# Performance work log

Measured on AMD Instinct MI355X. Metric: run time of the kernel, lower is better.

The kernel has to match this reference:

```python
import jax, jax.numpy as jnp
import numpy as np

N_NODES = 50000


def _gcn_layer(x, src, dst, W, b, inv_deg):
    # gather src features, scatter-add into dst, right-normalize, then dense transform
    agg = jax.ops.segment_sum(x[src], dst, num_segments=N_NODES)  # [N, F]
    h = agg * inv_deg[:, None]
    return h @ W + b


def setup_inputs() -> dict:
    key = jax.random.key(0)
    ks = jax.random.split(key, 6)
    E = 800000
    x = jax.random.normal(ks[0], (N_NODES, 128), dtype=jnp.float32)
    src = jax.random.randint(ks[1], (E,), 0, N_NODES, dtype=jnp.int64)
    dst = jax.random.randint(ks[2], (E,), 0, N_NODES, dtype=jnp.int64)
    W1 = jax.random.normal(ks[3], (128, 128), dtype=jnp.float32) * (1.0 / np.sqrt(128))
    b1 = jnp.zeros((128,), dtype=jnp.float32)
    W2 = jax.random.normal(ks[4], (128, 64), dtype=jnp.float32) * (1.0 / np.sqrt(128))
    b2 = jnp.zeros((64,), dtype=jnp.float32)
    return {"x": x, "src": src, "dst": dst, "W1": W1, "b1": b1, "W2": W2, "b2": b2}


def reference(x, src, dst, W1, b1, W2, b2):
    # in-degree, clamped to 1 (DGL norm='right')
    deg = jax.ops.segment_sum(jnp.ones_like(dst, dtype=x.dtype), dst, num_segments=N_NODES)
    inv_deg = 1.0 / jnp.maximum(deg, 1.0)
    h = _gcn_layer(x, src, dst, W1, b1, inv_deg)
    h = jax.nn.relu(h)  # Dropout in eval mode == identity
    out = _gcn_layer(h, src, dst, W2, b2, inv_deg)
    return out
```

## Files before the change

### kernel.cpp

```cpp
#include <hip/hip_runtime.h>


constexpr int NNODES = 50000;
constexpr int NEDGES = 800000;
constexpr int NBUCKETS = (NNODES + 255) / 256;
constexpr int ABLOCKS = 200;
constexpr int PER = (NEDGES + ABLOCKS - 1) / ABLOCKS;
constexpr int NB_CAST = NNODES / 16;
constexpr int NB_PREP = (128 * 128 + 64 * 128 + 255) / 256;

constexpr size_t SZ_ROWSTART = 50048;
constexpr size_t SZ_INVDEG   = 50048;
constexpr size_t SZ_H        = (size_t)ABLOCKS * 256;
constexpr size_t SZ_LOFS     = (size_t)ABLOCKS * 256;
constexpr size_t SZ_CSR      = NEDGES;
constexpr size_t SZ_TMP      = NEDGES;
constexpr size_t SZ_WT1      = 128 * 128 / 2;
constexpr size_t SZ_WT2      = 64 * 128 / 2;
constexpr size_t SZ_SCALEX   = 50048;
constexpr size_t SZ_XQ       = (size_t)NNODES * 128 / 4;
constexpr size_t SZ_AGGH     = (size_t)NNODES * 128 / 2;
constexpr size_t SZ_Y2H      = (size_t)NNODES * 64 / 2;

constexpr size_t OFF_ROWSTART = 0;
constexpr size_t OFF_INVDEG   = OFF_ROWSTART + SZ_ROWSTART;
constexpr size_t OFF_H        = OFF_INVDEG   + SZ_INVDEG;
constexpr size_t OFF_LOFS     = OFF_H        + SZ_H;
constexpr size_t OFF_CSR      = OFF_LOFS     + SZ_LOFS;
constexpr size_t OFF_TMP      = OFF_CSR      + SZ_CSR;
constexpr size_t OFF_WT1      = OFF_TMP      + SZ_TMP;
constexpr size_t OFF_WT2      = OFF_WT1      + SZ_WT1;
constexpr size_t OFF_SCALEX   = OFF_WT2      + SZ_WT2;
constexpr size_t OFF_XQ       = OFF_SCALEX   + SZ_SCALEX;
constexpr size_t OFF_AGGH     = OFF_XQ       + SZ_XQ;
constexpr size_t OFF_Y2H      = OFF_AGGH     + SZ_AGGH;
constexpr size_t WS_WORDS     = OFF_Y2H      + SZ_Y2H;
static_assert(WS_WORDS < 11452800, "exceeds r7-proven workspace size");

typedef unsigned short ushortv8 __attribute__((ext_vector_type(8)));
typedef short bf16x8 __attribute__((ext_vector_type(8)));
typedef float f32x4 __attribute__((ext_vector_type(4)));
typedef signed char charv8 __attribute__((ext_vector_type(8)));
typedef signed char charv16 __attribute__((ext_vector_type(16)));

static __device__ __forceinline__ unsigned short f2bf(float f) {
    unsigned u = __float_as_uint(f);
    u += 0x7fff + ((u >> 16) & 1);
    return (unsigned short)(u >> 16);
}
static __device__ __forceinline__ float bf2f(unsigned short h) {
    return __uint_as_float((unsigned)h << 16);
}

__global__ __launch_bounds__(256) void setup_kernel(
    const int* __restrict__ src, const int* __restrict__ dst,
    unsigned* __restrict__ tmp, int* __restrict__ H, int* __restrict__ LOFS,
    const float* __restrict__ x, signed char* __restrict__ xq,
    float* __restrict__ scaleX,
    const float* __restrict__ W1, const float* __restrict__ W2,
    unsigned short* __restrict__ Wt1, unsigned short* __restrict__ Wt2)
{
    const int blk = blockIdx.x;
    const int t = threadIdx.x;
    if (blk < ABLOCKS) {
        __shared__ int cnt[256];
        __shared__ int ofs[256];
        __shared__ int cur[256];
        cnt[t] = 0;
        __syncthreads();
        const int lo = blk * PER;
        const int hi = min(lo + PER, NEDGES);
        for (int i = lo + t; i < hi; i += 256)
            atomicAdd(&cnt[dst[i] >> 8], 1);
        __syncthreads();
        ofs[t] = cnt[t];
        __syncthreads();
        #pragma unroll
        for (int off = 1; off < 256; off <<= 1) {
            const int o = (t >= off) ? ofs[t - off] : 0;
            __syncthreads();
            ofs[t] += o;
            __syncthreads();
        }
        const int excl = ofs[t] - cnt[t];
        cur[t] = excl;
        H[blk * 256 + t] = cnt[t];
        LOFS[blk * 256 + t] = excl;
        __syncthreads();
        for (int i = lo + t; i < hi; i += 256) {
            const int d = dst[i];
            const unsigned pk = ((unsigned)src[i] << 8) | (unsigned)(d & 255);
            const int pos = lo + atomicAdd(&cur[d >> 8], 1);
            tmp[pos] = pk;
        }
    } else if (blk < ABLOCKS + NB_CAST) {
        const int lane = t & 63;
        const int wave = t >> 6;
        const int row = (blk - ABLOCKS) * 16 + wave * 4 + (lane >> 4);
        const int ls = lane & 15;
        const float4* px =
            reinterpret_cast<const float4*>(x + (size_t)row * 128 + ls * 8);
        const float4 a = px[0], b = px[1];
        float m = fmaxf(
            fmaxf(fmaxf(fabsf(a.x), fabsf(a.y)), fmaxf(fabsf(a.z), fabsf(a.w))),
            fmaxf(fmaxf(fabsf(b.x), fabsf(b.y)), fmaxf(fabsf(b.z), fabsf(b.w))));
        #pragma unroll
        for (int msk = 1; msk < 16; msk <<= 1)
            m = fmaxf(m, __shfl_xor(m, msk, 16));
        const float rs = (m > 0.f) ? 127.0f / m : 0.f;
        charv8 q;
        q[0] = (signed char)__float2int_rn(a.x * rs);
        q[1] = (signed char)__float2int_rn(a.y * rs);
        q[2] = (signed char)__float2int_rn(a.z * rs);
        q[3] = (signed char)__float2int_rn(a.w * rs);
        q[4] = (signed char)__float2int_rn(b.x * rs);
        q[5] = (signed char)__float2int_rn(b.y * rs);
        q[6] = (signed char)__float2int_rn(b.z * rs);
        q[7] = (signed char)__float2int_rn(b.w * rs);
        *reinterpret_cast<charv8*>(xq + (size_t)row * 128 + ls * 8) = q;
        if (ls == 0) scaleX[row] = (m > 0.f) ? m / 127.0f : 0.f;
    } else {
        const int i = (blk - ABLOCKS - NB_CAST) * 256 + t;
        if (i < 128 * 128) {
            const int n = i >> 7, k = i & 127;
            Wt1[i] = f2bf(W1[k * 128 + n]);
        } else if (i < 128 * 128 + 64 * 128) {
            const int j = i - 128 * 128;
            const int n = j >> 7, k = j & 127;
            Wt2[j] = f2bf(W2[k * 64 + n]);
        }
    }
}

__global__ __launch_bounds__(256) void partB_kernel(
    const unsigned* __restrict__ tmp, const int* __restrict__ H,
    const int* __restrict__ LOFS, int* __restrict__ csr,
    int* __restrict__ rowStart, float* __restrict__ inv_deg, int nNodes)
{
    __shared__ int cs[256];
    __shared__ int s[256];
    __shared__ int epfx[256];
    __shared__ int base[256];
    __shared__ int cnt[256];
    __shared__ int fill[256];
    const int b = blockIdx.x;
    const int t = threadIdx.x;

    int sum = 0;
    for (int w = 0; w < ABLOCKS; ++w) sum += H[w * 256 + t];
    cs[t] = sum;
    s[t] = sum;
    __syncthreads();
    #pragma unroll
    for (int off = 1; off < 256; off <<= 1) {
        const int o = (t >= off) ? s[t - off] : 0;
        __syncthreads();
        s[t] += o;
        __syncthreads();
    }
    const int gbase = s[b] - cs[b];
    const int total = cs[b];
    __syncthreads();

    const int hv = (t < ABLOCKS) ? H[t * 256 + b] : 0;
    s[t] = hv;
    if (t < ABLOCKS) base[t] = t * PER + LOFS[t * 256 + b];
    cnt[t] = 0;
    __syncthreads();
    #pragma unroll
    for (int off = 1; off < 256; off <<= 1) {
        const int o = (t >= off) ? s[t - off] : 0;
        __syncthreads();
        s[t] += o;
        __syncthreads();
    }
    epfx[t] = s[t] - hv;
    __syncthreads();

    for (int j = t; j < total; j += 256) {
        int loW = 0, hiW = ABLOCKS;
        while (hiW - loW > 1) {
            const int mid = (loW + hiW) >> 1;
            if (epfx[mid] <= j) loW = mid; else hiW = mid;
        }
        const unsigned p = tmp[base[loW] + (j - epfx[loW])];
        atomicAdd(&cnt[p & 255u], 1);
    }
    __syncthreads();
    s[t] = cnt[t];
    __syncthreads();
    #pragma unroll
    for (int off = 1; off < 256; off <<= 1) {
        const int o = (t >= off) ? s[t - off] : 0;
        __syncthreads();
        s[t] += o;
        __syncthreads();
    }
    const int excl = gbase + s[t] - cnt[t];
    const int node = b * 256 + t;
    if (node < nNodes) {
        rowStart[node] = excl;
        inv_deg[node] = 1.0f / fmaxf((float)cnt[t], 1.0f);
    }
    if (b == 0 && t == 0) rowStart[nNodes] = NEDGES;
    fill[t] = excl;
    __syncthreads();

    for (int j = t; j < total; j += 256) {
        int loW = 0, hiW = ABLOCKS;
        while (hiW - loW > 1) {
            const int mid = (loW + hiW) >> 1;
            if (epfx[mid] <= j) loW = mid; else hiW = mid;
        }
        const unsigned p = tmp[base[loW] + (j - epfx[loW])];
        const int pos = atomicAdd(&fill[p & 255u], 1);
        csr[pos] = (int)(p >> 8);
    }
}

__global__ __launch_bounds__(256) void gather_i8_kernel(
    const charv16* __restrict__ featq, const float* __restrict__ scaleX,
    const int* __restrict__ csr, const int* __restrict__ rowStart,
    ushortv8* __restrict__ aggH, int nNodes)
{
    constexpr int LPR = 8;
    constexpr int EPW = 8;
    const int wid = (blockIdx.x * 256 + threadIdx.x) >> 6;
    if (wid >= nNodes) return;
    const int lane = threadIdx.x & 63;
    const int eslot = lane / LPR;
    const int cg = lane % LPR;
    const int rs = rowStart[wid];
    const int re = rowStart[wid + 1];

    float acc0[16] = {}, acc1[16] = {};
    int j = rs + eslot;
    for (; j + EPW < re; j += 2 * EPW) {
        const int s0 = csr[j];
        const int s1 = csr[j + EPW];
        const charv16 q0 = featq[(size_t)s0 * 8 + cg];
        const charv16 q1 = featq[(size_t)s1 * 8 + cg];
        const float sc0 = scaleX[s0];
        const float sc1 = scaleX[s1];
        #pragma unroll
        for (int t = 0; t < 16; ++t) acc0[t] += (float)q0[t] * sc0;
        #pragma unroll
        for (int t = 0; t < 16; ++t) acc1[t] += (float)q1[t] * sc1;
    }
    if (j < re) {
        const int s0 = csr[j];
        const charv16 q0 = featq[(size_t)s0 * 8 + cg];
        const float sc0 = scaleX[s0];
        #pragma unroll
        for (int t = 0; t < 16; ++t) acc0[t] += (float)q0[t] * sc0;
    }
    #pragma unroll
    for (int t = 0; t < 16; ++t) acc0[t] += acc1[t];

    #pragma unroll
    for (int off = LPR; off < 64; off <<= 1) {
        #pragma unroll
        for (int t = 0; t < 16; ++t) acc0[t] += __shfl_down(acc0[t], off, 64);
    }

    if (lane < LPR) {
        ushortv8 o0, o1;
        #pragma unroll
        for (int t = 0; t < 8; ++t) {
            o0[t] = f2bf(acc0[t]);
            o1[t] = f2bf(acc0[t + 8]);
        }
        aggH[(size_t)wid * 16 + cg * 2] = o0;
        aggH[(size_t)wid * 16 + cg * 2 + 1] = o1;
    }
}

template<int F, bool EPI>
__global__ __launch_bounds__(256) void gather_bf16_kernel(
    const ushortv8* __restrict__ feat, const int* __restrict__ csr,
    const int* __restrict__ rowStart, const float* __restrict__ inv_deg,
    const float* __restrict__ bias, float* __restrict__ outv, int nNodes)
{
    constexpr int LPR = F / 8;
    constexpr int EPW = 64 / LPR;
    const int wid = (blockIdx.x * 256 + threadIdx.x) >> 6;
    if (wid >= nNodes) return;
    const int lane = threadIdx.x & 63;
    const int eslot = lane / LPR;
    const int cg = lane % LPR;
    const int rs = rowStart[wid];
    const int re = rowStart[wid + 1];

    float acc0[8] = {}, acc1[8] = {};
    int j = rs + eslot;
    for (; j + EPW < re; j += 2 * EPW) {
        const int s0 = csr[j];
        const int s1 = csr[j + EPW];
        const ushortv8 v0 = feat[(size_t)s0 * LPR + cg];
        const ushortv8 v1 = feat[(size_t)s1 * LPR + cg];
        #pragma unroll
        for (int t = 0; t < 8; ++t) acc0[t] += bf2f(v0[t]);
        #pragma unroll
        for (int t = 0; t < 8; ++t) acc1[t] += bf2f(v1[t]);
    }
    if (j < re) {
        const int s0 = csr[j];
        const ushortv8 v0 = feat[(size_t)s0 * LPR + cg];
        #pragma unroll
        for (int t = 0; t < 8; ++t) acc0[t] += bf2f(v0[t]);
    }
    #pragma unroll
    for (int t = 0; t < 8; ++t) acc0[t] += acc1[t];

    #pragma unroll
    for (int off = LPR; off < 64; off <<= 1) {
        #pragma unroll
        for (int t = 0; t < 8; ++t) acc0[t] += __shfl_down(acc0[t], off, 64);
    }

    if (lane < LPR) {
        if constexpr (EPI) {
            const float s = inv_deg[wid];
            #pragma unroll
            for (int t = 0; t < 8; ++t) acc0[t] = acc0[t] * s + bias[cg * 8 + t];
        }
        float* o = outv + (size_t)wid * F + cg * 8;
        *reinterpret_cast<float4*>(o) =
            make_float4(acc0[0], acc0[1], acc0[2], acc0[3]);
        *reinterpret_cast<float4*>(o + 4) =
            make_float4(acc0[4], acc0[5], acc0[6], acc0[7]);
    }
}

__global__ __launch_bounds__(256) void mfma_fused_kernel(
    const ushortv8* __restrict__ A,
    const float* __restrict__ inv_deg,
    const ushortv8* __restrict__ Wt1,
    const float* __restrict__ b1,
    const ushortv8* __restrict__ Wt2,
    unsigned short* __restrict__ y2h,
    int nrows)
{
    constexpr int LDK = 136;
    __shared__ alignas(16) unsigned short lwt1[128][LDK];
    __shared__ alignas(16) unsigned short lwt2[64][LDK];
    __shared__ alignas(16) unsigned short la[64][LDK];

    const int row0 = blockIdx.x * 64;
    const int t = threadIdx.x;

    for (int i = t; i < 128 * 16; i += 256) {
        const int r = i >> 4, c = i & 15;
        *reinterpret_cast<ushortv8*>(&lwt1[r][c * 8]) = Wt1[i];
    }
    for (int i = t; i < 64 * 16; i += 256) {
        const int r = i >> 4, c = i & 15;
        *reinterpret_cast<ushortv8*>(&lwt2[r][c * 8]) = Wt2[i];
    }
    for (int i = t; i < 64 * 16; i += 256) {
        const int r = i >> 4, c = i & 15;
        const int row = row0 + r;
        ushortv8 v = {};
        if (row < nrows) {
            v = A[(size_t)row * 16 + c];
            const float s = inv_deg[row];
            #pragma unroll
            for (int jj = 0; jj < 8; ++jj) v[jj] = f2bf(bf2f(v[jj]) * s);
        }
        *reinterpret_cast<ushortv8*>(&la[r][c * 8]) = v;
    }
    __syncthreads();

    const int wave = t >> 6, lane = t & 63;
    const int m = lane & 15, kg = lane >> 4;

    f32x4 acc1[8] = {};
    #pragma unroll
    for (int kk = 0; kk < 4; ++kk) {
        const bf16x8 af =
            *reinterpret_cast<const bf16x8*>(&la[wave * 16 + m][kk * 32 + kg * 8]);
        #pragma unroll
        for (int n = 0; n < 8; ++n) {
            const bf16x8 bf =
                *reinterpret_cast<const bf16x8*>(&lwt1[n * 16 + m][kk * 32 + kg * 8]);
            acc1[n] = __builtin_amdgcn_mfma_f32_16x16x32_bf16(af, bf, acc1[n], 0, 0, 0);
        }
    }
    #pragma unroll
    for (int n = 0; n < 8; ++n) {
        const float bv = b1[n * 16 + m];
        #pragma unroll
        for (int q = 0; q < 4; ++q) {
            const int r = wave * 16 + kg * 4 + q;
            la[r][n * 16 + m] = f2bf(fmaxf(acc1[n][q] + bv, 0.f));
        }
    }
    __syncthreads();

    f32x4 acc2[4] = {};
    #pragma unroll
    for (int kk = 0; kk < 4; ++kk) {
        const bf16x8 af =
            *reinterpret_cast<const bf16x8*>(&la[wave * 16 + m][kk * 32 + kg * 8]);
        #pragma unroll
        for (int n = 0; n < 4; ++n) {
            const bf16x8 bf =
                *reinterpret_cast<const bf16x8*>(&lwt2[n * 16 + m][kk * 32 + kg * 8]);
            acc2[n] = __builtin_amdgcn_mfma_f32_16x16x32_bf16(af, bf, acc2[n], 0, 0, 0);
        }
    }
    __syncthreads();
    #pragma unroll
    for (int n = 0; n < 4; ++n) {
        #pragma unroll
        for (int q = 0; q < 4; ++q) {
            const int r = wave * 16 + kg * 4 + q;
            la[r][n * 16 + m] = f2bf(acc2[n][q]);
        }
    }
    __syncthreads();
    for (int i = t; i < 64 * 8; i += 256) {
        const int r = i >> 3, c = i & 7;
        const int row = row0 + r;
        if (row < nrows)
            *reinterpret_cast<ushortv8*>(&y2h[(size_t)row * 64 + c * 8]) =
                *reinterpret_cast<const ushortv8*>(&la[r][c * 8]);
    }
}

extern "C" void kernel_launch(void* const* d_in, const int* in_sizes, int n_in,
                              void* d_out, int out_size, void* d_ws, size_t ws_size,
                              hipStream_t stream)
{
    const float* x   = (const float*)d_in[0];
    const int*   src = (const int*)d_in[1];
    const int*   dst = (const int*)d_in[2];
    const float* W1  = (const float*)d_in[3];
    const float* b1  = (const float*)d_in[4];
    const float* W2  = (const float*)d_in[5];
    const float* b2  = (const float*)d_in[6];
    float* out = (float*)d_out;

    float* ws  = (float*)d_ws;
    int*   wsi = (int*)d_ws;
    int*            rowStart = wsi + OFF_ROWSTART;
    float*          invdeg   = ws  + OFF_INVDEG;
    int*            H        = wsi + OFF_H;
    int*            LOFS     = wsi + OFF_LOFS;
    int*            csr      = wsi + OFF_CSR;
    unsigned*       tmp      = (unsigned*)(wsi + OFF_TMP);
    unsigned short* Wt1      = (unsigned short*)(wsi + OFF_WT1);
    unsigned short* Wt2      = (unsigned short*)(wsi + OFF_WT2);
    float*          scaleX   = ws  + OFF_SCALEX;
    signed char*    xq       = (signed char*)(wsi + OFF_XQ);
    ushortv8*       aggH     = (ushortv8*)(wsi + OFF_AGGH);
    unsigned short* y2h      = (unsigned short*)(wsi + OFF_Y2H);

    setup_kernel<<<ABLOCKS + NB_CAST + NB_PREP, 256, 0, stream>>>(
        src, dst, tmp, H, LOFS, x, xq, scaleX, W1, W2, Wt1, Wt2);

    partB_kernel<<<NBUCKETS, 256, 0, stream>>>(
        tmp, H, LOFS, csr, rowStart, invdeg, NNODES);

    gather_i8_kernel<<<(NNODES + 3) / 4, 256, 0, stream>>>(
        (const charv16*)xq, scaleX, csr, rowStart, aggH, NNODES);

    mfma_fused_kernel<<<(NNODES + 63) / 64, 256, 0, stream>>>(
        aggH, invdeg, (const ushortv8*)Wt1, b1, (const ushortv8*)Wt2,
        y2h, NNODES);

    gather_bf16_kernel<64, true><<<(NNODES + 3) / 4, 256, 0, stream>>>(
        (const ushortv8*)y2h, csr, rowStart, invdeg, b2, out, NNODES);
}
```

Before: 124.6 us.

## Fuse int8 neighbor gather into the two-layer MFMA kernel, drop aggH buffer

The first-layer gather now runs inside the MFMA kernel. Each 256-thread block aggregates its 64 destination rows in place, one row per wave per pass for 16 passes, and writes them already scaled by inverse degree into shared memory. This removes the bf16 aggH round trip through global memory and one kernel launch. The weight tiles are no longer staged in shared memory; MFMA B operands are read straight from global Wt1/Wt2, which cuts LDS use and may raise occupancy. In exchange, the gather now runs with 782 blocks instead of 12500 and serialises 16 rows per wave, so latency hiding and load balance across the irregular graph may suffer.

```diff
diff --git a/kernel.cpp b/kernel.cpp
--- a/kernel.cpp
+++ b/kernel.cpp
@@ -19,7 +19,6 @@
 constexpr size_t SZ_WT2      = 64 * 128 / 2;
 constexpr size_t SZ_SCALEX   = 50048;
 constexpr size_t SZ_XQ       = (size_t)NNODES * 128 / 4;
-constexpr size_t SZ_AGGH     = (size_t)NNODES * 128 / 2;
 constexpr size_t SZ_Y2H      = (size_t)NNODES * 64 / 2;
 
 constexpr size_t OFF_ROWSTART = 0;
@@ -32,8 +31,7 @@
 constexpr size_t OFF_WT2      = OFF_WT1      + SZ_WT1;
 constexpr size_t OFF_SCALEX   = OFF_WT2      + SZ_WT2;
 constexpr size_t OFF_XQ       = OFF_SCALEX   + SZ_SCALEX;
-constexpr size_t OFF_AGGH     = OFF_XQ       + SZ_XQ;
-constexpr size_t OFF_Y2H      = OFF_AGGH     + SZ_AGGH;
+constexpr size_t OFF_Y2H      = OFF_XQ       + SZ_XQ;
 constexpr size_t WS_WORDS     = OFF_Y2H      + SZ_Y2H;
 static_assert(WS_WORDS < 11452800, "exceeds r7-proven workspace size");
 
@@ -218,60 +216,128 @@
     }
 }
 
-__global__ __launch_bounds__(256) void gather_i8_kernel(
+__global__ __launch_bounds__(256) void gat_gemm_kernel(
     const charv16* __restrict__ featq, const float* __restrict__ scaleX,
     const int* __restrict__ csr, const int* __restrict__ rowStart,
-    ushortv8* __restrict__ aggH, int nNodes)
+    const float* __restrict__ inv_deg,
+    const unsigned short* __restrict__ Wt1,
+    const float* __restrict__ b1,
+    const unsigned short* __restrict__ Wt2,
+    unsigned short* __restrict__ y2h,
+    int nNodes)
 {
-    constexpr int LPR = 8;
-    constexpr int EPW = 8;
-    const int wid = (blockIdx.x * 256 + threadIdx.x) >> 6;
-    if (wid >= nNodes) return;
-    const int lane = threadIdx.x & 63;
-    const int eslot = lane / LPR;
-    const int cg = lane % LPR;
-    const int rs = rowStart[wid];
-    const int re = rowStart[wid + 1];
-
-    float acc0[16] = {}, acc1[16] = {};
-    int j = rs + eslot;
-    for (; j + EPW < re; j += 2 * EPW) {
-        const int s0 = csr[j];
-        const int s1 = csr[j + EPW];
-        const charv16 q0 = featq[(size_t)s0 * 8 + cg];
-        const charv16 q1 = featq[(size_t)s1 * 8 + cg];
-        const float sc0 = scaleX[s0];
-        const float sc1 = scaleX[s1];
-        #pragma unroll
-        for (int t = 0; t < 16; ++t) acc0[t] += (float)q0[t] * sc0;
-        #pragma unroll
-        for (int t = 0; t < 16; ++t) acc1[t] += (float)q1[t] * sc1;
-    }
-    if (j < re) {
-        const int s0 = csr[j];
-        const charv16 q0 = featq[(size_t)s0 * 8 + cg];
-        const float sc0 = scaleX[s0];
-        #pragma unroll
-        for (int t = 0; t < 16; ++t) acc0[t] += (float)q0[t] * sc0;
-    }
-    #pragma unroll
-    for (int t = 0; t < 16; ++t) acc0[t] += acc1[t];
-
-    #pragma unroll
-    for (int off = LPR; off < 64; off <<= 1) {
-        #pragma unroll
-        for (int t = 0; t < 16; ++t) acc0[t] += __shfl_down(acc0[t], off, 64);
-    }
-
-    if (lane < LPR) {
-        ushortv8 o0, o1;
-        #pragma unroll
-        for (int t = 0; t < 8; ++t) {
-            o0[t] = f2bf(acc0[t]);
-            o1[t] = f2bf(acc0[t + 8]);
-        }
-        aggH[(size_t)wid * 16 + cg * 2] = o0;
-        aggH[(size_t)wid * 16 + cg * 2 + 1] = o1;
+    constexpr int LDK = 136;
+    __shared__ alignas(16) unsigned short la[64][LDK];
+
+    const int row0 = blockIdx.x * 64;
+    const int t = threadIdx.x;
+    const int wave = t >> 6, lane = t & 63;
+
+    const int eslot = lane >> 3;
+    const int cg = lane & 7;
+    for (int p = 0; p < 16; ++p) {
+        const int r = p * 4 + wave;
+        const int node = row0 + r;
+        float acc0[16] = {}, acc1[16] = {};
+        if (node < nNodes) {
+            const int rs = rowStart[node];
+            const int re = rowStart[node + 1];
+            int j = rs + eslot;
+            for (; j + 8 < re; j += 16) {
+                const int s0 = csr[j];
+                const int s1 = csr[j + 8];
+                const charv16 q0 = featq[(size_t)s0 * 8 + cg];
+                const charv16 q1 = featq[(size_t)s1 * 8 + cg];
+                const float sc0 = scaleX[s0];
+                const float sc1 = scaleX[s1];
+                #pragma unroll
+                for (int k = 0; k < 16; ++k) acc0[k] += (float)q0[k] * sc0;
+                #pragma unroll
+                for (int k = 0; k < 16; ++k) acc1[k] += (float)q1[k] * sc1;
+            }
+            if (j < re) {
+                const int s0 = csr[j];
+                const charv16 q0 = featq[(size_t)s0 * 8 + cg];
+                const float sc0 = scaleX[s0];
+                #pragma unroll
+                for (int k = 0; k < 16; ++k) acc0[k] += (float)q0[k] * sc0;
+            }
+        }
+        #pragma unroll
+        for (int k = 0; k < 16; ++k) acc0[k] += acc1[k];
+        #pragma unroll
+        for (int off = 8; off < 64; off <<= 1) {
+            #pragma unroll
+            for (int k = 0; k < 16; ++k)
+                acc0[k] += __shfl_down(acc0[k], off, 64);
+        }
+        if (lane < 8) {
+            const float s = (node < nNodes) ? inv_deg[node] : 0.f;
+            ushortv8 o0, o1;
+            #pragma unroll
+            for (int k = 0; k < 8; ++k) {
+                o0[k] = f2bf(acc0[k] * s);
+                o1[k] = f2bf(acc0[k + 8] * s);
+            }
+            *reinterpret_cast<ushortv8*>(&la[r][cg * 16]) = o0;
+            *reinterpret_cast<ushortv8*>(&la[r][cg * 16 + 8]) = o1;
+        }
+    }
+    __syncthreads();
+
+    const int m = lane & 15, kg = lane >> 4;
+
+    f32x4 acc1g[8] = {};
+    #pragma unroll
+    for (int kk = 0; kk < 4; ++kk) {
+        const bf16x8 af =
+            *reinterpret_cast<const bf16x8*>(&la[wave * 16 + m][kk * 32 + kg * 8]);
+        #pragma unroll
+        for (int n = 0; n < 8; ++n) {
+            const bf16x8 bf = *reinterpret_cast<const bf16x8*>(
+                &Wt1[((size_t)(n * 16 + m) << 7) + kk * 32 + kg * 8]);
+            acc1g[n] = __builtin_amdgcn_mfma_f32_16x16x32_bf16(af, bf, acc1g[n], 0, 0, 0);
+        }
+    }
+    #pragma unroll
+    for (int n = 0; n < 8; ++n) {
+        const float bv = b1[n * 16 + m];
+        #pragma unroll
+        for (int q = 0; q < 4; ++q) {
+            const int r = wave * 16 + kg * 4 + q;
+            la[r][n * 16 + m] = f2bf(fmaxf(acc1g[n][q] + bv, 0.f));
+        }
+    }
+    __syncthreads();
+
+    f32x4 acc2g[4] = {};
+    #pragma unroll
+    for (int kk = 0; kk < 4; ++kk) {
+        const bf16x8 af =
+            *reinterpret_cast<const bf16x8*>(&la[wave * 16 + m][kk * 32 + kg * 8]);
+        #pragma unroll
+        for (int n = 0; n < 4; ++n) {
+            const bf16x8 bf = *reinterpret_cast<const bf16x8*>(
+                &Wt2[((size_t)(n * 16 + m) << 7) + kk * 32 + kg * 8]);
+            acc2g[n] = __builtin_amdgcn_mfma_f32_16x16x32_bf16(af, bf, acc2g[n], 0, 0, 0);
+        }
+    }
+    __syncthreads();
+    #pragma unroll
+    for (int n = 0; n < 4; ++n) {
+        #pragma unroll
+        for (int q = 0; q < 4; ++q) {
+            const int r = wave * 16 + kg * 4 + q;
+            la[r][n * 16 + m] = f2bf(acc2g[n][q]);
+        }
+    }
+    __syncthreads();
+    for (int i = t; i < 64 * 8; i += 256) {
+        const int r = i >> 3, c = i & 7;
+        const int row = row0 + r;
+        if (row < nNodes)
+            *reinterpret_cast<ushortv8*>(&y2h[(size_t)row * 64 + c * 8]) =
+                *reinterpret_cast<const ushortv8*>(&la[r][c * 8]);
     }
 }
 
@@ -332,102 +398,6 @@
     }
 }
 
-__global__ __launch_bounds__(256) void mfma_fused_kernel(
-    const ushortv8* __restrict__ A,
-    const float* __restrict__ inv_deg,
-    const ushortv8* __restrict__ Wt1,
-    const float* __restrict__ b1,
-    const ushortv8* __restrict__ Wt2,
-    unsigned short* __restrict__ y2h,
-    int nrows)
-{
-    constexpr int LDK = 136;
-    __shared__ alignas(16) unsigned short lwt1[128][LDK];
-    __shared__ alignas(16) unsigned short lwt2[64][LDK];
-    __shared__ alignas(16) unsigned short la[64][LDK];
-
-    const int row0 = blockIdx.x * 64;
-    const int t = threadIdx.x;
-
-    for (int i = t; i < 128 * 16; i += 256) {
-        const int r = i >> 4, c = i & 15;
-        *reinterpret_cast<ushortv8*>(&lwt1[r][c * 8]) = Wt1[i];
-    }
-    for (int i = t; i < 64 * 16; i += 256) {
-        const int r = i >> 4, c = i & 15;
-        *reinterpret_cast<ushortv8*>(&lwt2[r][c * 8]) = Wt2[i];
-    }
-    for (int i = t; i < 64 * 16; i += 256) {
-        const int r = i >> 4, c = i & 15;
-        const int row = row0 + r;
-        ushortv8 v = {};
-        if (row < nrows) {
-            v = A[(size_t)row * 16 + c];
-            const float s = inv_deg[row];
-            #pragma unroll
-            for (int jj = 0; jj < 8; ++jj) v[jj] = f2bf(bf2f(v[jj]) * s);
-        }
-        *reinterpret_cast<ushortv8*>(&la[r][c * 8]) = v;
-    }
-    __syncthreads();
-
-    const int wave = t >> 6, lane = t & 63;
-    const int m = lane & 15, kg = lane >> 4;
-
-    f32x4 acc1[8] = {};
-    #pragma unroll
-    for (int kk = 0; kk < 4; ++kk) {
-        const bf16x8 af =
-            *reinterpret_cast<const bf16x8*>(&la[wave * 16 + m][kk * 32 + kg * 8]);
-        #pragma unroll
-        for (int n = 0; n < 8; ++n) {
-            const bf16x8 bf =
-                *reinterpret_cast<const bf16x8*>(&lwt1[n * 16 + m][kk * 32 + kg * 8]);
-            acc1[n] = __builtin_amdgcn_mfma_f32_16x16x32_bf16(af, bf, acc1[n], 0, 0, 0);
-        }
-    }
-    #pragma unroll
-    for (int n = 0; n < 8; ++n) {
-        const float bv = b1[n * 16 + m];
-        #pragma unroll
-        for (int q = 0; q < 4; ++q) {
-            const int r = wave * 16 + kg * 4 + q;
-            la[r][n * 16 + m] = f2bf(fmaxf(acc1[n][q] + bv, 0.f));
-        }
-    }
-    __syncthreads();
-
-    f32x4 acc2[4] = {};
-    #pragma unroll
-    for (int kk = 0; kk < 4; ++kk) {
-        const bf16x8 af =
-            *reinterpret_cast<const bf16x8*>(&la[wave * 16 + m][kk * 32 + kg * 8]);
-        #pragma unroll
-        for (int n = 0; n < 4; ++n) {
-            const bf16x8 bf =
-                *reinterpret_cast<const bf16x8*>(&lwt2[n * 16 + m][kk * 32 + kg * 8]);
-            acc2[n] = __builtin_amdgcn_mfma_f32_16x16x32_bf16(af, bf, acc2[n], 0, 0, 0);
-        }
-    }
-    __syncthreads();
-    #pragma unroll
-    for (int n = 0; n < 4; ++n) {
-        #pragma unroll
-        for (int q = 0; q < 4; ++q) {
-            const int r = wave * 16 + kg * 4 + q;
-            la[r][n * 16 + m] = f2bf(acc2[n][q]);
-        }
-    }
-    __syncthreads();
-    for (int i = t; i < 64 * 8; i += 256) {
-        const int r = i >> 3, c = i & 7;
-        const int row = row0 + r;
-        if (row < nrows)
-            *reinterpret_cast<ushortv8*>(&y2h[(size_t)row * 64 + c * 8]) =
-                *reinterpret_cast<const ushortv8*>(&la[r][c * 8]);
-    }
-}
-
 extern "C" void kernel_launch(void* const* d_in, const int* in_sizes, int n_in,
                               void* d_out, int out_size, void* d_ws, size_t ws_size,
                               hipStream_t stream)
@@ -453,7 +423,6 @@
     unsigned short* Wt2      = (unsigned short*)(wsi + OFF_WT2);
     float*          scaleX   = ws  + OFF_SCALEX;
     signed char*    xq       = (signed char*)(wsi + OFF_XQ);
-    ushortv8*       aggH     = (ushortv8*)(wsi + OFF_AGGH);
     unsigned short* y2h      = (unsigned short*)(wsi + OFF_Y2H);
 
     setup_kernel<<<ABLOCKS + NB_CAST + NB_PREP, 256, 0, stream>>>(
@@ -462,12 +431,9 @@
     partB_kernel<<<NBUCKETS, 256, 0, stream>>>(
         tmp, H, LOFS, csr, rowStart, invdeg, NNODES);
 
-    gather_i8_kernel<<<(NNODES + 3) / 4, 256, 0, stream>>>(
-        (const charv16*)xq, scaleX, csr, rowStart, aggH, NNODES);
-
-    mfma_fused_kernel<<<(NNODES + 63) / 64, 256, 0, stream>>>(
-        aggH, invdeg, (const ushortv8*)Wt1, b1, (const ushortv8*)Wt2,
-        y2h, NNODES);
+    gat_gemm_kernel<<<(NNODES + 63) / 64, 256, 0, stream>>>(
+        (const charv16*)xq, scaleX, csr, rowStart, invdeg,
+        Wt1, b1, Wt2, y2h, NNODES);
 
     gather_bf16_kernel<64, true><<<(NNODES + 3) / 4, 256, 0, stream>>>(
         (const ushortv8*)y2h, csr, rowStart, invdeg, b2, out, NNODES);
```

Measured after the change: 149.4 us. +20.0%, slower.
